# Optimization experiments

Hardware: AMD Instinct MI355X
Metric: run time of the kernel (lower is better)

Reference implementation:

```python
import jax, jax.numpy as jnp
import numpy as np

N_NODES = 50000
N_EDGES = 800000
IN_DIM = 256
H1 = 512
H2 = 128


def _gcn_conv(x, W, b, row, col, ew, n_nodes):
    """PyG GCNConv with edge_weight: linear (no bias) -> add self-loops ->
    symmetric normalization -> weighted scatter-add -> + bias."""
    xw = x @ W  # [N, out]
    loop = jnp.arange(n_nodes, dtype=row.dtype)
    row_f = jnp.concatenate([row, loop])
    col_f = jnp.concatenate([col, loop])
    ew_f = jnp.concatenate([ew, jnp.ones((n_nodes,), dtype=ew.dtype)])
    deg = jax.ops.segment_sum(ew_f, col_f, num_segments=n_nodes)  # in-degree
    dinv = jnp.where(deg > 0, jax.lax.rsqrt(jnp.where(deg > 0, deg, 1.0)), 0.0)
    norm = dinv[row_f] * ew_f * dinv[col_f]  # [E+N]
    msg = norm[:, None] * xw[row_f]          # [E+N, out] gather
    out = jax.ops.segment_sum(msg, col_f, num_segments=n_nodes)  # scatter-add
    return out + b


def _prelu(x, alpha):
    return jnp.where(x >= 0, x, alpha * x)


def setup_inputs() -> dict:
    key = jax.random.key(0)
    ks = jax.random.split(key, 6)
    x = jax.random.normal(ks[0], (N_NODES, IN_DIM), dtype=jnp.float32)
    edge_index = jax.random.randint(ks[1], (2, N_EDGES), 0, N_NODES, dtype=jnp.int32)
    edge_attr = jax.random.uniform(ks[2], (N_EDGES,), dtype=jnp.float32)
    W1 = jax.random.normal(ks[3], (IN_DIM, H1), dtype=jnp.float32) / np.sqrt(IN_DIM)
    b1 = jnp.zeros((H1,), dtype=jnp.float32)
    W2 = jax.random.normal(ks[4], (H1, H2), dtype=jnp.float32) / np.sqrt(H1)
    b2 = jnp.zeros((H2,), dtype=jnp.float32)
    alpha = jnp.ones((1,), dtype=jnp.float32) * 0.25  # nn.PReLU default init
    return {"x": x, "edge_attr": edge_attr, "W1": W1, "b1": b1,
            "W2": W2, "b2": b2, "alpha": alpha, "edge_index": edge_index}


def reference(x, edge_attr, W1, b1, W2, b2, alpha, edge_index):
    row, col = edge_index[0], edge_index[1]
    # Dropout treated as identity (deterministic eval-mode reference).
    feat1 = _prelu(_gcn_conv(x, W1, b1, row, col, edge_attr, N_NODES), alpha)
    feat2 = _prelu(_gcn_conv(feat1, W2, b2, row, col, edge_attr, N_NODES), alpha)
    return feat2
```

## Files before the change

kernel.cpp:

```cpp
#include <hip/hip_runtime.h>

#define N_NODES 50000
#define N_EDGES 800000
#define IN_DIM  256
#define H1      512
#define H2      128

typedef __attribute__((ext_vector_type(8))) short  short8v;
typedef __attribute__((ext_vector_type(4))) float  float4v;
typedef __attribute__((ext_vector_type(4))) unsigned short ushort4v;

__device__ __forceinline__ void split_bf16(float v, unsigned short& h, unsigned short& l) {
    unsigned u = __builtin_bit_cast(unsigned, v);
    unsigned hr = (u + 0x7FFFu + ((u >> 16) & 1u)) >> 16;
    float hf = __builtin_bit_cast(float, hr << 16);
    float lf = v - hf;
    unsigned ul = __builtin_bit_cast(unsigned, lf);
    unsigned lr = (ul + 0x7FFFu + ((ul >> 16) & 1u)) >> 16;
    h = (unsigned short)hr; l = (unsigned short)lr;
}


__global__ void init_kernel(float* deg, int* cnt, int n) {
    int i = blockIdx.x * blockDim.x + threadIdx.x;
    if (i < n) { deg[i] = 1.0f; cnt[i] = 0; }
}

__global__ void edge_deg_kernel(const int* __restrict__ col, const float* __restrict__ ew,
                                float* deg, int* cnt, int ne) {
    int e = blockIdx.x * blockDim.x + threadIdx.x;
    if (e < ne) {
        int c = col[e];
        atomicAdd(&deg[c], ew[e]);
        atomicAdd(&cnt[c], 1);
    }
}

__global__ void dinv_kernel(const float* __restrict__ deg, float* dinv, int n) {
    int i = blockIdx.x * blockDim.x + threadIdx.x;
    if (i < n) dinv[i] = rsqrtf(deg[i]);
}

__global__ void scan_block_kernel(const int* __restrict__ cnt, int* __restrict__ part,
                                  int* __restrict__ bsum, int n) {
    __shared__ int s[256];
    int tid = threadIdx.x;
    int i = blockIdx.x * 256 + tid;
    int v = (i < n) ? cnt[i] : 0;
    s[tid] = v; __syncthreads();
#pragma unroll
    for (int d = 1; d < 256; d <<= 1) {
        int t = (tid >= d) ? s[tid - d] : 0; __syncthreads();
        s[tid] += t; __syncthreads();
    }
    if (i < n) part[i] = s[tid] - v;
    if (tid == 255) bsum[blockIdx.x] = s[255];
}

__global__ void scan_tops_kernel(const int* __restrict__ bsum, int* __restrict__ boff, int nb) {
    __shared__ int s[256];
    int tid = threadIdx.x;
    int v = (tid < nb) ? bsum[tid] : 0;
    s[tid] = v; __syncthreads();
#pragma unroll
    for (int d = 1; d < 256; d <<= 1) {
        int t = (tid >= d) ? s[tid - d] : 0; __syncthreads();
        s[tid] += t; __syncthreads();
    }
    if (tid < nb) boff[tid] = s[tid] - v;
}

__global__ void scan_add_kernel(const int* __restrict__ part, const int* __restrict__ boff,
                                int* __restrict__ ptr, int* __restrict__ fill, int n) {
    int i = blockIdx.x * 256 + threadIdx.x;
    if (i < n) {
        int p = part[i] + boff[blockIdx.x];
        ptr[i] = p; fill[i] = p;
    }
    if (i == 0) ptr[n] = N_EDGES;
}

__global__ void scatter_kernel(const int* __restrict__ row, const int* __restrict__ col,
                               const float* __restrict__ ew, const float* __restrict__ dinv,
                               int* fill, int* srcs, float* coef, int ne) {
    int e = blockIdx.x * blockDim.x + threadIdx.x;
    if (e < ne) {
        int r = row[e], c = col[e];
        int pos = atomicAdd(&fill[c], 1);
        srcs[pos] = r;
        coef[pos] = dinv[r] * ew[e] * dinv[c];
    }
}

__global__ void convw_kernel(const float* __restrict__ W, unsigned short* __restrict__ Wh,
                             unsigned short* __restrict__ Wl, int K, int N) {
    int idx = blockIdx.x * 256 + threadIdx.x;
    if (idx < N * K) {
        int n = idx / K, k = idx % K;
        unsigned short h, l;
        split_bf16(W[(size_t)k * N + n], h, l);
        Wh[idx] = h; Wl[idx] = l;
    }
}


__global__ __launch_bounds__(256) void agg256_kernel(
        const float* __restrict__ x, const float* __restrict__ dinv,
        const int* __restrict__ ptr, const int* __restrict__ srcs,
        const float* __restrict__ coef,
        unsigned short* __restrict__ out_h, unsigned short* __restrict__ out_l) {
    int wv = threadIdx.x >> 6, lane = threadIdx.x & 63;
    int node = blockIdx.x * 4 + wv;
    if (node >= N_NODES) return;
    const float4* x4 = (const float4*)x;
    float di = dinv[node];
    float s = di * di;
    float4 v = x4[node * 64 + lane];
    float ax = v.x * s, ay = v.y * s, az = v.z * s, aw = v.w * s;
    int j = ptr[node], e1 = ptr[node + 1];
    for (; j + 1 < e1; j += 2) {
        int s0 = srcs[j], s1 = srcs[j + 1];
        float c0 = coef[j], c1 = coef[j + 1];
        float4 u0 = x4[s0 * 64 + lane];
        float4 u1 = x4[s1 * 64 + lane];
        ax += c0 * u0.x + c1 * u1.x;
        ay += c0 * u0.y + c1 * u1.y;
        az += c0 * u0.z + c1 * u1.z;
        aw += c0 * u0.w + c1 * u1.w;
    }
    if (j < e1) {
        int s0 = srcs[j];
        float c0 = coef[j];
        float4 u0 = x4[s0 * 64 + lane];
        ax += c0 * u0.x; ay += c0 * u0.y; az += c0 * u0.z; aw += c0 * u0.w;
    }
    unsigned short hx, lx, hy, ly, hz, lz, hw, lw;
    split_bf16(ax, hx, lx);
    split_bf16(ay, hy, ly);
    split_bf16(az, hz, lz);
    split_bf16(aw, hw, lw);
    ushort4v h4 = {hx, hy, hz, hw};
    ushort4v l4 = {lx, ly, lz, lw};
    *(ushort4v*)(out_h + (size_t)node * IN_DIM + lane * 4) = h4;
    *(ushort4v*)(out_l + (size_t)node * IN_DIM + lane * 4) = l4;
}

__global__ __launch_bounds__(256) void agg128_epi_kernel(
        const float* __restrict__ xw, const float* __restrict__ dinv,
        const int* __restrict__ ptr, const int* __restrict__ srcs,
        const float* __restrict__ coef, const float* __restrict__ b2,
        const float* __restrict__ alphap, float* __restrict__ out) {
    int wv = threadIdx.x >> 6, lane = threadIdx.x & 63;
    int node = blockIdx.x * 4 + wv;
    if (node >= N_NODES) return;
    const float2* x2 = (const float2*)xw;
    float di = dinv[node];
    float s = di * di;
    float2 v = x2[node * 64 + lane];
    float ax = v.x * s, ay = v.y * s;
    int j = ptr[node], e1 = ptr[node + 1];
    for (; j + 1 < e1; j += 2) {
        int s0 = srcs[j], s1 = srcs[j + 1];
        float c0 = coef[j], c1 = coef[j + 1];
        float2 u0 = x2[s0 * 64 + lane];
        float2 u1 = x2[s1 * 64 + lane];
        ax += c0 * u0.x + c1 * u1.x;
        ay += c0 * u0.y + c1 * u1.y;
    }
    if (j < e1) {
        int s0 = srcs[j];
        float c0 = coef[j];
        float2 u0 = x2[s0 * 64 + lane];
        ax += c0 * u0.x; ay += c0 * u0.y;
    }
    float alpha = alphap[0];
    float2 b = ((const float2*)b2)[lane];
    ax += b.x; ay += b.y;
    ax = (ax >= 0.f) ? ax : alpha * ax;
    ay = (ay >= 0.f) ? ay : alpha * ay;
    ((float2*)out)[node * 64 + lane] = make_float2(ax, ay);
}


__device__ __forceinline__ int swz(int row, int k ) {
    return ((row << 7) + (k << 1)) ^ ((row & 7) << 4);
}

__device__ __forceinline__ void stage_plane(const unsigned short* __restrict__ g,
                                            unsigned short* l, int srow, int sk, bool ok) {
#pragma unroll
    for (int j = 0; j < 4; ++j) {
        short8v v = {0,0,0,0,0,0,0,0};
        if (ok) v = *(const short8v*)(g + sk + j * 8);
        *(short8v*)((char*)l + swz(srow, sk + j * 8)) = v;
    }
}

template <int MODE>
__global__ __launch_bounds__(256, 2) void gemm_mfma_kernel(
        const unsigned short* __restrict__ A_hi, const unsigned short* __restrict__ A_lo,
        const unsigned short* __restrict__ B_hi, const unsigned short* __restrict__ B_lo,
        const float* __restrict__ bias, const float* __restrict__ alphap,
        unsigned short* __restrict__ Oh, unsigned short* __restrict__ Ol,
        float* __restrict__ Of, int M, int N, int K) {
    __shared__ unsigned short smem[4][8192];
    unsigned short* Ah = smem[0];
    unsigned short* Al = smem[1];
    unsigned short* Bh = smem[2];
    unsigned short* Bl = smem[3];

    const int tid  = threadIdx.x;
    const int lane = tid & 63, wave = tid >> 6;
    const int wm = wave >> 1, wn = wave & 1;
    const int lr = lane & 15, lk = (lane >> 4) << 3;
    const int srow = tid >> 1, sk = (tid & 1) << 5;

    const int m0 = blockIdx.y * 128, n0 = blockIdx.x * 128;

    float4v acc[4][4] = {};

    const bool arow_ok = (m0 + srow) < M;
    const unsigned short* gAh = A_hi + (size_t)(m0 + srow) * K;
    const unsigned short* gAl = A_lo + (size_t)(m0 + srow) * K;
    const unsigned short* gBh = B_hi + (size_t)(n0 + srow) * K;
    const unsigned short* gBl = B_lo + (size_t)(n0 + srow) * K;

    for (int k0 = 0; k0 < K; k0 += 64) {
        stage_plane(gAh + k0, Ah, srow, sk, arow_ok);
        stage_plane(gAl + k0, Al, srow, sk, arow_ok);
        stage_plane(gBh + k0, Bh, srow, sk, true);
        stage_plane(gBl + k0, Bl, srow, sk, true);
        __syncthreads();
#pragma unroll
        for (int q = 0; q < 2; ++q) {
            short8v ah[4], al[4], bh[4], bl[4];
#pragma unroll
            for (int i = 0; i < 4; ++i) {
                ah[i] = *(const short8v*)((const char*)Ah + swz(wm * 64 + i * 16 + lr, q * 32 + lk));
                al[i] = *(const short8v*)((const char*)Al + swz(wm * 64 + i * 16 + lr, q * 32 + lk));
                bh[i] = *(const short8v*)((const char*)Bh + swz(wn * 64 + i * 16 + lr, q * 32 + lk));
                bl[i] = *(const short8v*)((const char*)Bl + swz(wn * 64 + i * 16 + lr, q * 32 + lk));
            }
#pragma unroll
            for (int mi = 0; mi < 4; ++mi)
#pragma unroll
                for (int ni = 0; ni < 4; ++ni) {
                    acc[mi][ni] = __builtin_amdgcn_mfma_f32_16x16x32_bf16(ah[mi], bh[ni], acc[mi][ni], 0, 0, 0);
                    acc[mi][ni] = __builtin_amdgcn_mfma_f32_16x16x32_bf16(ah[mi], bl[ni], acc[mi][ni], 0, 0, 0);
                    acc[mi][ni] = __builtin_amdgcn_mfma_f32_16x16x32_bf16(al[mi], bh[ni], acc[mi][ni], 0, 0, 0);
                }
        }
        __syncthreads();
    }

    const float alpha = (MODE == 1) ? alphap[0] : 0.f;
#pragma unroll
    for (int mi = 0; mi < 4; ++mi) {
        int grow_base = m0 + wm * 64 + mi * 16 + (lane >> 4) * 4;
#pragma unroll
        for (int ni = 0; ni < 4; ++ni) {
            int gcol = n0 + wn * 64 + ni * 16 + lr;
#pragma unroll
            for (int r = 0; r < 4; ++r) {
                int grow = grow_base + r;
                if (grow < M) {
                    float v = acc[mi][ni][r];
                    if (MODE == 1) {
                        v += bias[gcol];
                        v = (v >= 0.f) ? v : alpha * v;
                        unsigned short h, l;
                        split_bf16(v, h, l);
                        Oh[(size_t)grow * N + gcol] = h;
                        Ol[(size_t)grow * N + gcol] = l;
                    } else {
                        Of[(size_t)grow * N + gcol] = v;
                    }
                }
            }
        }
    }
}


extern "C" void kernel_launch(void* const* d_in, const int* in_sizes, int n_in,
                              void* d_out, int out_size, void* d_ws, size_t ws_size,
                              hipStream_t stream) {
    const float* x     = (const float*)d_in[0];
    const float* eattr = (const float*)d_in[1];
    const float* W1    = (const float*)d_in[2];
    const float* b1    = (const float*)d_in[3];
    const float* W2    = (const float*)d_in[4];
    const float* b2    = (const float*)d_in[5];
    const float* alpha = (const float*)d_in[6];
    const int*   eidx  = (const int*)d_in[7];
    const int* row = eidx;
    const int* col = eidx + N_EDGES;
    float* out = (float*)d_out;

    float* ws_f = (float*)d_ws;
    size_t off = 0;
    float* deg   = ws_f + off; off += N_NODES;
    float* dinv  = ws_f + off; off += N_NODES;
    float* coef  = ws_f + off; off += N_EDGES;
    unsigned short* aggx_h = (unsigned short*)(ws_f + off); off += (size_t)N_NODES * IN_DIM / 2;
    unsigned short* aggx_l = (unsigned short*)(ws_f + off); off += (size_t)N_NODES * IN_DIM / 2;
    float* xw2 = (float*)aggx_h;
    unsigned short* feat1_h = (unsigned short*)(ws_f + off); off += (size_t)N_NODES * H1 / 2;
    unsigned short* feat1_l = (unsigned short*)(ws_f + off); off += (size_t)N_NODES * H1 / 2;
    unsigned short* W1t_h = (unsigned short*)(ws_f + off); off += (size_t)IN_DIM * H1 / 2;
    unsigned short* W1t_l = (unsigned short*)(ws_f + off); off += (size_t)IN_DIM * H1 / 2;
    unsigned short* W2t_h = (unsigned short*)(ws_f + off); off += (size_t)H1 * H2 / 2;
    unsigned short* W2t_l = (unsigned short*)(ws_f + off); off += (size_t)H1 * H2 / 2;
    int* cnt  = (int*)(ws_f + off); off += N_NODES;
    int* ptr  = (int*)(ws_f + off); off += N_NODES + 1;
    int* fill = (int*)(ws_f + off); off += N_NODES;
    int* part = (int*)(ws_f + off); off += N_NODES;
    int* bsum = (int*)(ws_f + off); off += 256;
    int* boff = (int*)(ws_f + off); off += 256;
    int* srcs = (int*)(ws_f + off); off += N_EDGES;

    const int nodeBlocks = (N_NODES + 255) / 256;
    const int edgeBlocks = (N_EDGES + 255) / 256;

    convw_kernel<<<(IN_DIM * H1 + 255) / 256, 256, 0, stream>>>(W1, W1t_h, W1t_l, IN_DIM, H1);
    convw_kernel<<<(H1 * H2 + 255) / 256, 256, 0, stream>>>(W2, W2t_h, W2t_l, H1, H2);

    init_kernel<<<nodeBlocks, 256, 0, stream>>>(deg, cnt, N_NODES);
    edge_deg_kernel<<<edgeBlocks, 256, 0, stream>>>(col, eattr, deg, cnt, N_EDGES);
    dinv_kernel<<<nodeBlocks, 256, 0, stream>>>(deg, dinv, N_NODES);
    scan_block_kernel<<<nodeBlocks, 256, 0, stream>>>(cnt, part, bsum, N_NODES);
    scan_tops_kernel<<<1, 256, 0, stream>>>(bsum, boff, nodeBlocks);
    scan_add_kernel<<<nodeBlocks, 256, 0, stream>>>(part, boff, ptr, fill, N_NODES);
    scatter_kernel<<<edgeBlocks, 256, 0, stream>>>(row, col, eattr, dinv, fill, srcs, coef, N_EDGES);

    agg256_kernel<<<(N_NODES + 3) / 4, 256, 0, stream>>>(x, dinv, ptr, srcs, coef, aggx_h, aggx_l);
    {
        dim3 grid(H1 / 128, (N_NODES + 127) / 128);
        gemm_mfma_kernel<1><<<grid, 256, 0, stream>>>(aggx_h, aggx_l, W1t_h, W1t_l,
                                                      b1, alpha, feat1_h, feat1_l, nullptr,
                                                      N_NODES, H1, IN_DIM);
    }

    {
        dim3 grid(H2 / 128, (N_NODES + 127) / 128);
        gemm_mfma_kernel<0><<<grid, 256, 0, stream>>>(feat1_h, feat1_l, W2t_h, W2t_l,
                                                      nullptr, nullptr, nullptr, nullptr, xw2,
                                                      N_NODES, H2, H1);
    }
    agg128_epi_kernel<<<(N_NODES + 3) / 4, 256, 0, stream>>>(xw2, dinv, ptr, srcs, coef, b2, alpha, out);
}
```

Before: 554.7 us.

## Pack CSR edges as int2, unroll aggregation by four, stage GEMM tiles via global_load_lds

The scatter kernel now writes each edge's source index and normalized weight as one interleaved int2 record, replacing the separate srcs and coef arrays. Both aggregation kernels read these records and unroll the neighbor loop by four, so each edge needs one load and more gathers are in flight at once. The GEMM tile staging switches from register-staged vector copies to direct global-to-LDS loads, with the k-chunk XOR permutation matching the existing swizzled layout. The row bounds check on the A tile is dropped, so the last M tile reads past the logical end of the activation buffers into adjacent workspace.

```diff
diff --git a/kernel.cpp b/kernel.cpp
--- a/kernel.cpp
+++ b/kernel.cpp
@@ -82,13 +82,13 @@
 
 __global__ void scatter_kernel(const int* __restrict__ row, const int* __restrict__ col,
                                const float* __restrict__ ew, const float* __restrict__ dinv,
-                               int* fill, int* srcs, float* coef, int ne) {
+                               int* fill, int2* __restrict__ edges, int ne) {
     int e = blockIdx.x * blockDim.x + threadIdx.x;
     if (e < ne) {
         int r = row[e], c = col[e];
         int pos = atomicAdd(&fill[c], 1);
-        srcs[pos] = r;
-        coef[pos] = dinv[r] * ew[e] * dinv[c];
+        float w = dinv[r] * ew[e] * dinv[c];
+        edges[pos] = make_int2(r, __float_as_int(w));
     }
 }
 
@@ -106,8 +106,7 @@
 
 __global__ __launch_bounds__(256) void agg256_kernel(
         const float* __restrict__ x, const float* __restrict__ dinv,
-        const int* __restrict__ ptr, const int* __restrict__ srcs,
-        const float* __restrict__ coef,
+        const int* __restrict__ ptr, const int2* __restrict__ edges,
         unsigned short* __restrict__ out_h, unsigned short* __restrict__ out_l) {
     int wv = threadIdx.x >> 6, lane = threadIdx.x & 63;
     int node = blockIdx.x * 4 + wv;
@@ -118,20 +117,23 @@
     float4 v = x4[node * 64 + lane];
     float ax = v.x * s, ay = v.y * s, az = v.z * s, aw = v.w * s;
     int j = ptr[node], e1 = ptr[node + 1];
-    for (; j + 1 < e1; j += 2) {
-        int s0 = srcs[j], s1 = srcs[j + 1];
-        float c0 = coef[j], c1 = coef[j + 1];
-        float4 u0 = x4[s0 * 64 + lane];
-        float4 u1 = x4[s1 * 64 + lane];
-        ax += c0 * u0.x + c1 * u1.x;
-        ay += c0 * u0.y + c1 * u1.y;
-        az += c0 * u0.z + c1 * u1.z;
-        aw += c0 * u0.w + c1 * u1.w;
-    }
-    if (j < e1) {
-        int s0 = srcs[j];
-        float c0 = coef[j];
-        float4 u0 = x4[s0 * 64 + lane];
+    for (; j + 3 < e1; j += 4) {
+        int2 e0 = edges[j], e1_ = edges[j + 1], e2 = edges[j + 2], e3 = edges[j + 3];
+        float4 u0 = x4[e0.x * 64 + lane];
+        float4 u1 = x4[e1_.x * 64 + lane];
+        float4 u2 = x4[e2.x * 64 + lane];
+        float4 u3 = x4[e3.x * 64 + lane];
+        float c0 = __int_as_float(e0.y), c1 = __int_as_float(e1_.y);
+        float c2 = __int_as_float(e2.y), c3 = __int_as_float(e3.y);
+        ax += c0 * u0.x + c1 * u1.x + c2 * u2.x + c3 * u3.x;
+        ay += c0 * u0.y + c1 * u1.y + c2 * u2.y + c3 * u3.y;
+        az += c0 * u0.z + c1 * u1.z + c2 * u2.z + c3 * u3.z;
+        aw += c0 * u0.w + c1 * u1.w + c2 * u2.w + c3 * u3.w;
+    }
+    for (; j < e1; ++j) {
+        int2 e0 = edges[j];
+        float c0 = __int_as_float(e0.y);
+        float4 u0 = x4[e0.x * 64 + lane];
         ax += c0 * u0.x; ay += c0 * u0.y; az += c0 * u0.z; aw += c0 * u0.w;
     }
     unsigned short hx, lx, hy, ly, hz, lz, hw, lw;
@@ -147,9 +149,9 @@
 
 __global__ __launch_bounds__(256) void agg128_epi_kernel(
         const float* __restrict__ xw, const float* __restrict__ dinv,
-        const int* __restrict__ ptr, const int* __restrict__ srcs,
-        const float* __restrict__ coef, const float* __restrict__ b2,
-        const float* __restrict__ alphap, float* __restrict__ out) {
+        const int* __restrict__ ptr, const int2* __restrict__ edges,
+        const float* __restrict__ b2, const float* __restrict__ alphap,
+        float* __restrict__ out) {
     int wv = threadIdx.x >> 6, lane = threadIdx.x & 63;
     int node = blockIdx.x * 4 + wv;
     if (node >= N_NODES) return;
@@ -159,18 +161,21 @@
     float2 v = x2[node * 64 + lane];
     float ax = v.x * s, ay = v.y * s;
     int j = ptr[node], e1 = ptr[node + 1];
-    for (; j + 1 < e1; j += 2) {
-        int s0 = srcs[j], s1 = srcs[j + 1];
-        float c0 = coef[j], c1 = coef[j + 1];
-        float2 u0 = x2[s0 * 64 + lane];
-        float2 u1 = x2[s1 * 64 + lane];
-        ax += c0 * u0.x + c1 * u1.x;
-        ay += c0 * u0.y + c1 * u1.y;
-    }
-    if (j < e1) {
-        int s0 = srcs[j];
-        float c0 = coef[j];
-        float2 u0 = x2[s0 * 64 + lane];
+    for (; j + 3 < e1; j += 4) {
+        int2 e0 = edges[j], e1_ = edges[j + 1], e2 = edges[j + 2], e3 = edges[j + 3];
+        float2 u0 = x2[e0.x * 64 + lane];
+        float2 u1 = x2[e1_.x * 64 + lane];
+        float2 u2 = x2[e2.x * 64 + lane];
+        float2 u3 = x2[e3.x * 64 + lane];
+        float c0 = __int_as_float(e0.y), c1 = __int_as_float(e1_.y);
+        float c2 = __int_as_float(e2.y), c3 = __int_as_float(e3.y);
+        ax += c0 * u0.x + c1 * u1.x + c2 * u2.x + c3 * u3.x;
+        ay += c0 * u0.y + c1 * u1.y + c2 * u2.y + c3 * u3.y;
+    }
+    for (; j < e1; ++j) {
+        int2 e0 = edges[j];
+        float c0 = __int_as_float(e0.y);
+        float2 u0 = x2[e0.x * 64 + lane];
         ax += c0 * u0.x; ay += c0 * u0.y;
     }
     float alpha = alphap[0];
@@ -186,13 +191,22 @@
     return ((row << 7) + (k << 1)) ^ ((row & 7) << 4);
 }
 
-__device__ __forceinline__ void stage_plane(const unsigned short* __restrict__ g,
-                                            unsigned short* l, int srow, int sk, bool ok) {
-#pragma unroll
-    for (int j = 0; j < 4; ++j) {
-        short8v v = {0,0,0,0,0,0,0,0};
-        if (ok) v = *(const short8v*)(g + sk + j * 8);
-        *(short8v*)((char*)l + swz(srow, sk + j * 8)) = v;
+__device__ __forceinline__ void gload16(const void* g, void* l) {
+    __builtin_amdgcn_global_load_lds(
+        (const __attribute__((address_space(1))) unsigned int*)g,
+        (__attribute__((address_space(3))) unsigned int*)l, 16, 0, 0);
+}
+
+__device__ __forceinline__ void stage_plane_async(
+        const unsigned short* __restrict__ gbase,
+        unsigned short* lds, int K, int grow0, int k0, int wave, int lane) {
+    int r8 = lane >> 3;
+    int kk = k0 + (((lane & 7) ^ r8) << 3);
+#pragma unroll
+    for (int t = 0; t < 4; ++t) {
+        int rowblk = wave * 32 + t * 8;
+        const unsigned short* g = gbase + (size_t)(grow0 + rowblk + r8) * K + kk;
+        gload16(g, lds + (size_t)rowblk * 64);
     }
 }
 
@@ -213,23 +227,16 @@
     const int lane = tid & 63, wave = tid >> 6;
     const int wm = wave >> 1, wn = wave & 1;
     const int lr = lane & 15, lk = (lane >> 4) << 3;
-    const int srow = tid >> 1, sk = (tid & 1) << 5;
 
     const int m0 = blockIdx.y * 128, n0 = blockIdx.x * 128;
 
     float4v acc[4][4] = {};
 
-    const bool arow_ok = (m0 + srow) < M;
-    const unsigned short* gAh = A_hi + (size_t)(m0 + srow) * K;
-    const unsigned short* gAl = A_lo + (size_t)(m0 + srow) * K;
-    const unsigned short* gBh = B_hi + (size_t)(n0 + srow) * K;
-    const unsigned short* gBl = B_lo + (size_t)(n0 + srow) * K;
-
     for (int k0 = 0; k0 < K; k0 += 64) {
-        stage_plane(gAh + k0, Ah, srow, sk, arow_ok);
-        stage_plane(gAl + k0, Al, srow, sk, arow_ok);
-        stage_plane(gBh + k0, Bh, srow, sk, true);
-        stage_plane(gBl + k0, Bl, srow, sk, true);
+        stage_plane_async(A_hi, Ah, K, m0, k0, wave, lane);
+        stage_plane_async(A_lo, Al, K, m0, k0, wave, lane);
+        stage_plane_async(B_hi, Bh, K, n0, k0, wave, lane);
+        stage_plane_async(B_lo, Bl, K, n0, k0, wave, lane);
         __syncthreads();
 #pragma unroll
         for (int q = 0; q < 2; ++q) {
@@ -301,7 +308,7 @@
     size_t off = 0;
     float* deg   = ws_f + off; off += N_NODES;
     float* dinv  = ws_f + off; off += N_NODES;
-    float* coef  = ws_f + off; off += N_EDGES;
+    int2*  edges = (int2*)(ws_f + off); off += (size_t)2 * N_EDGES;
     unsigned short* aggx_h = (unsigned short*)(ws_f + off); off += (size_t)N_NODES * IN_DIM / 2;
     unsigned short* aggx_l = (unsigned short*)(ws_f + off); off += (size_t)N_NODES * IN_DIM / 2;
     float* xw2 = (float*)aggx_h;
@@ -317,7 +324,6 @@
     int* part = (int*)(ws_f + off); off += N_NODES;
     int* bsum = (int*)(ws_f + off); off += 256;
     int* boff = (int*)(ws_f + off); off += 256;
-    int* srcs = (int*)(ws_f + off); off += N_EDGES;
 
     const int nodeBlocks = (N_NODES + 255) / 256;
     const int edgeBlocks = (N_EDGES + 255) / 256;
@@ -331,9 +337,9 @@
     scan_block_kernel<<<nodeBlocks, 256, 0, stream>>>(cnt, part, bsum, N_NODES);
     scan_tops_kernel<<<1, 256, 0, stream>>>(bsum, boff, nodeBlocks);
     scan_add_kernel<<<nodeBlocks, 256, 0, stream>>>(part, boff, ptr, fill, N_NODES);
-    scatter_kernel<<<edgeBlocks, 256, 0, stream>>>(row, col, eattr, dinv, fill, srcs, coef, N_EDGES);
-
-    agg256_kernel<<<(N_NODES + 3) / 4, 256, 0, stream>>>(x, dinv, ptr, srcs, coef, aggx_h, aggx_l);
+    scatter_kernel<<<edgeBlocks, 256, 0, stream>>>(row, col, eattr, dinv, fill, edges, N_EDGES);
+
+    agg256_kernel<<<(N_NODES + 3) / 4, 256, 0, stream>>>(x, dinv, ptr, edges, aggx_h, aggx_l);
     {
         dim3 grid(H1 / 128, (N_NODES + 127) / 128);
         gemm_mfma_kernel<1><<<grid, 256, 0, stream>>>(aggx_h, aggx_l, W1t_h, W1t_l,
@@ -347,5 +353,5 @@
                                                       nullptr, nullptr, nullptr, nullptr, xw2,
                                                       N_NODES, H2, H1);
     }
-    agg128_epi_kernel<<<(N_NODES + 3) / 4, 256, 0, stream>>>(xw2, dinv, ptr, srcs, coef, b2, alpha, out);
-}
+    agg128_epi_kernel<<<(N_NODES + 3) / 4, 256, 0, stream>>>(xw2, dinv, ptr, edges, b2, alpha, out);
+}
```

New measurement: 525.2 us. -5.3%, faster.
